# Performance work log

Hardware: AMD Instinct MI355X
Metric: run time of the kernel (lower is better)

## Reference

```python
import jax, jax.numpy as jnp
import numpy as np

N = 32768
LAYERS = [3, 128, 128, 128, 128, 128, 128, 128, 128, 2]


def setup_inputs() -> dict:
    key = jax.random.key(0)
    keys = jax.random.split(key, 3 + 2 * (len(LAYERS) - 1))
    inp = {
        "x": jax.random.normal(keys[0], (N, 1), jnp.float32),
        "y": jax.random.normal(keys[1], (N, 1), jnp.float32),
        "t": jax.random.normal(keys[2], (N, 1), jnp.float32),
    }
    # torch.nn.Linear default init: U(-1/sqrt(fan_in), 1/sqrt(fan_in))
    for i in range(len(LAYERS) - 1):
        bound = 1.0 / np.sqrt(LAYERS[i])
        inp[f"W{i}"] = jax.random.uniform(keys[3 + 2 * i], (LAYERS[i], LAYERS[i + 1]), jnp.float32, -bound, bound)
        inp[f"b{i}"] = jax.random.uniform(keys[4 + 2 * i], (LAYERS[i + 1],), jnp.float32, -bound, bound)
    inp["lam1"] = jnp.asarray([1.0], jnp.float32)
    inp["lam2"] = jnp.asarray([0.01], jnp.float32)
    return inp


def _pinn(x, y, t, params, lam1, lam2):
    pts = jnp.concatenate([x, y, t], axis=1)  # [N,3], columns = (x, y, t)

    def psi(pt):  # pt: [3] -> scalar stream function (output column 0)
        h = pt
        for W, b in params:
            h = jnp.tanh(h @ W + b)  # note: tanh applied to last layer too, as in source
        return h[0]

    g_fn = jax.grad(psi)          # [3]        d psi / d(x,y,t)
    H_fn = jax.jacfwd(g_fn)       # [3,3]      second derivatives
    T_fn = jax.jacfwd(H_fn)       # [3,3,3]    third derivatives
    g, H, T = jax.vmap(lambda pt: (g_fn(pt), H_fn(pt), T_fn(pt)))(pts)

    col = lambda a: a[:, None]  # [N] -> [N,1]
    u = col(g[:, 1])            # u = psi_y
    v = col(-g[:, 0])           # v = -psi_x
    u_x, u_y, u_t = col(H[:, 1, 0]), col(H[:, 1, 1]), col(H[:, 1, 2])
    v_x, v_y, v_t = col(-H[:, 0, 0]), col(-H[:, 0, 1]), col(-H[:, 0, 2])
    u_xx, u_yy = col(T[:, 1, 0, 0]), col(T[:, 1, 1, 1])
    v_xx, v_yy = col(-T[:, 0, 0, 0]), col(-T[:, 0, 1, 1])

    f_u = u_t + lam1 * (u * u_x + v * u_y) - lam2 * (u_xx + u_yy)
    f_v = v_t + lam1 * (u * v_x + v * v_y) - lam2 * (v_xx + v_yy)
    return u, v, f_u, f_v


def reference(x, y, t, W0, b0, W1, b1, W2, b2, W3, b3, W4, b4, W5, b5, W6, b6, W7, b7, W8, b8, lam1, lam2):
    params = [(W0, b0), (W1, b1), (W2, b2), (W3, b3), (W4, b4), (W5, b5), (W6, b6), (W7, b7), (W8, b8)]
    return _pinn(x, y, t, params, lam1, lam2)
```

## Files before the change

### kernel.cpp

```cpp
#include <hip/hip_runtime.h>
#include <math.h>

#define NPTS 32768
#define HID  128
#define PPB  4
#define NCH  13
#define KB   32

typedef __attribute__((ext_vector_type(8))) _Float16 f16x8;
typedef __attribute__((ext_vector_type(4))) float f32x4;

struct PinnArgs {
  const float* x; const float* y; const float* t;
  const float* W[9]; const float* b[9];
  const float* lam1; const float* lam2;
  float* out;
  const _Float16* wt;
};

struct PrepArgs { const float* W[7]; _Float16* out; };

__device__ __forceinline__ void compose13(const float z[NCH], float o[NCH]) {
  const float v  = tanhf(z[0]);
  const float f1 = 1.f - v * v;
  const float f2 = -2.f * v * f1;
  const float f3 = f1 * (4.f * v * v - 2.f * f1);
  const float gx = z[1], gy = z[2], gt = z[3];
  const float hxx = z[4], hxy = z[5], hxt = z[6], hyy = z[7], hyt = z[8];
  o[0] = v;
  o[1] = f1 * gx; o[2] = f1 * gy; o[3] = f1 * gt;
  o[4] = f2 * gx * gx + f1 * hxx;
  o[5] = f2 * gx * gy + f1 * hxy;
  o[6] = f2 * gx * gt + f1 * hxt;
  o[7] = f2 * gy * gy + f1 * hyy;
  o[8] = f2 * gy * gt + f1 * hyt;
  o[9]  = f3 * gx * gx * gx + f2 * (3.f * hxx * gx)            + f1 * z[9];
  o[10] = f3 * gx * gx * gy + f2 * (hxx * gy + 2.f * hxy * gx) + f1 * z[10];
  o[11] = f3 * gx * gy * gy + f2 * (2.f * hxy * gy + hyy * gx) + f1 * z[11];
  o[12] = f3 * gy * gy * gy + f2 * (3.f * hyy * gy)            + f1 * z[12];
}

__global__ __launch_bounds__(256) void prep_w16(PrepArgs P) {
  const int idx = blockIdx.x * 256 + threadIdx.x;
  if (idx >= 7 * 16384) return;
  const int L = idx >> 14;
  const int r = idx & 16383;
  const int n = r & 127;
  const int k = r >> 7;
  const float w = P.W[L][k * HID + n];
  const _Float16 hi = (_Float16)w;
  const _Float16 lo = (_Float16)(w - (float)hi);
  P.out[(size_t)(L * 2 + 0) * 16384 + n * 128 + k] = hi;
  P.out[(size_t)(L * 2 + 1) * 16384 + n * 128 + k] = lo;
}

__global__ __launch_bounds__(256, 3) void pinn_mfma(PinnArgs A) {
  __shared__ _Float16 Ah[64][136];
  __shared__ _Float16 Al[64][136];
  __shared__ float    Zh[64][68];
  const int tid  = threadIdx.x;
  const int wave = tid >> 6;
  const int lane = tid & 63;
  const int kg   = lane >> 4;
  const int lr   = lane & 15;
  const int pbase = blockIdx.x * PPB;

  if (tid < 136) {
#pragma unroll
    for (int pp = 0; pp < PPB; ++pp)
#pragma unroll
      for (int c = NCH; c < 16; ++c) {
        Ah[pp * 16 + c][tid] = (_Float16)0.f;
        Al[pp * 16 + c][tid] = (_Float16)0.f;
      }
  }

  for (int t = tid; t < PPB * HID; t += 256) {
    const int p = t >> 7, j = t & 127;
    const int gp = pbase + p;
    const float xv = A.x[gp], yv = A.y[gp], tv = A.t[gp];
    const float wx = A.W[0][j], wy = A.W[0][HID + j], wz = A.W[0][2 * HID + j];
    float z[NCH], o[NCH];
    z[0] = fmaf(wx, xv, fmaf(wy, yv, fmaf(wz, tv, A.b[0][j])));
    z[1] = wx; z[2] = wy; z[3] = wz;
#pragma unroll
    for (int c = 4; c < NCH; ++c) z[c] = 0.f;
    compose13(z, o);
#pragma unroll
    for (int c = 0; c < NCH; ++c) {
      const _Float16 hi = (_Float16)o[c];
      Ah[p * 16 + c][j] = hi;
      Al[p * 16 + c][j] = (_Float16)(o[c] - (float)hi);
    }
  }
  __syncthreads();

#pragma unroll 1
  for (int L = 1; L <= 7; ++L) {
    const _Float16* __restrict__ WH = A.wt + (size_t)(L - 1) * 2 * 16384;
    const _Float16* __restrict__ WL = WH + 16384;
    f16x8 bh[2][4], bl[2][4];
#pragma unroll
    for (int nt = 0; nt < 2; ++nt) {
      const int col = wave * 32 + nt * 16 + lr;
#pragma unroll
      for (int ks = 0; ks < 4; ++ks) {
        const int k0 = ks * 32 + kg * 8;
        bh[nt][ks] = *(const f16x8*)(WH + col * 128 + k0);
        bl[nt][ks] = *(const f16x8*)(WL + col * 128 + k0);
      }
    }
    f32x4 acc[4][2];
#pragma unroll
    for (int m = 0; m < 4; ++m)
#pragma unroll
      for (int nt = 0; nt < 2; ++nt) acc[m][nt] = (f32x4)(0.f);

#pragma unroll
    for (int ks = 0; ks < 4; ++ks) {
      const int k0 = ks * 32 + kg * 8;
#pragma unroll
      for (int m = 0; m < 4; ++m) {
        const int row = m * 16 + lr;
        const f16x8 ah = *(const f16x8*)&Ah[row][k0];
        const f16x8 al = *(const f16x8*)&Al[row][k0];
#pragma unroll
        for (int nt = 0; nt < 2; ++nt) {
          acc[m][nt] = __builtin_amdgcn_mfma_f32_16x16x32_f16(ah, bh[nt][ks], acc[m][nt], 0, 0, 0);
          acc[m][nt] = __builtin_amdgcn_mfma_f32_16x16x32_f16(ah, bl[nt][ks], acc[m][nt], 0, 0, 0);
          acc[m][nt] = __builtin_amdgcn_mfma_f32_16x16x32_f16(al, bh[nt][ks], acc[m][nt], 0, 0, 0);
        }
      }
    }

    const float* __restrict__ bb = A.b[L];
#pragma unroll
    for (int nt = 0; nt < 2; ++nt) {
#pragma unroll
      for (int m = 0; m < 4; ++m)
        *(f32x4*)&Zh[wave * 16 + lr][m * 16 + kg * 4] = acc[m][nt];
      __syncthreads();

      {
        const int p = wave;
        const int s = lane;
        const int j = ((s >> 4) << 5) + nt * 16 + (s & 15);
        float zf[16], o[NCH];
#pragma unroll
        for (int q = 0; q < 4; ++q)
          ((f32x4*)zf)[q] = *(const f32x4*)&Zh[s][p * 16 + 4 * q];
        zf[0] += bb[j];
        compose13(zf, o);
#pragma unroll
        for (int c = 0; c < NCH; ++c) {
          const _Float16 hi = (_Float16)o[c];
          Ah[p * 16 + c][j] = hi;
          Al[p * 16 + c][j] = (_Float16)(o[c] - (float)hi);
        }
      }
      __syncthreads();
    }
  }

  {
    const int p = wave, gp = pbase + p;
    const float w0 = A.W[8][2 * lane];
    const float w1 = A.W[8][2 * (lane + 64)];
    float zc[NCH];
#pragma unroll
    for (int c = 0; c < NCH; ++c) {
      const int rr = p * 16 + c;
      const float s0 = (float)Ah[rr][lane]      + (float)Al[rr][lane];
      const float s1 = (float)Ah[rr][lane + 64] + (float)Al[rr][lane + 64];
      zc[c] = fmaf(s0, w0, s1 * w1);
    }
#pragma unroll
    for (int off = 32; off; off >>= 1) {
#pragma unroll
      for (int c = 0; c < NCH; ++c) zc[c] += __shfl_xor(zc[c], off, 64);
    }
    if (lane == 0) {
      zc[0] += A.b[8][0];
      float o[NCH];
      compose13(zc, o);
      const float u  =  o[2];
      const float vv = -o[1];
      const float ux =  o[5],  uy =  o[7],  ut =  o[8];
      const float vx = -o[4],  vy = -o[5],  vt = -o[6];
      const float uxx =  o[10], uyy =  o[12];
      const float vxx = -o[9],  vyy = -o[11];
      const float l1 = A.lam1[0], l2 = A.lam2[0];
      const float fu = ut + l1 * (u * ux + vv * uy) - l2 * (uxx + uyy);
      const float fv = vt + l1 * (u * vx + vv * vy) - l2 * (vxx + vyy);
      A.out[gp]            = u;
      A.out[NPTS + gp]     = vv;
      A.out[2 * NPTS + gp] = fu;
      A.out[3 * NPTS + gp] = fv;
    }
  }
}

__device__ __forceinline__ void compose20(const float z[20], float o[20]) {
  const float v  = tanhf(z[0]);
  const float f1 = 1.f - v * v;
  const float f2 = -2.f * v * f1;
  const float f3 = f1 * (4.f * v * v - 2.f * f1);
  const float gx = z[1], gy = z[2], gt = z[3];
  const float hxx = z[4], hxy = z[5], hxz = z[6], hyy = z[7], hyz = z[8], hzz = z[9];
  o[0] = v;
  o[1] = f1 * gx; o[2] = f1 * gy; o[3] = f1 * gt;
  o[4] = f2 * gx * gx + f1 * hxx;
  o[5] = f2 * gx * gy + f1 * hxy;
  o[6] = f2 * gx * gt + f1 * hxz;
  o[7] = f2 * gy * gy + f1 * hyy;
  o[8] = f2 * gy * gt + f1 * hyz;
  o[9] = f2 * gt * gt + f1 * hzz;
  o[10] = f3 * gx * gx * gx + f2 * (3.f * hxx * gx)                 + f1 * z[10];
  o[11] = f3 * gx * gx * gy + f2 * (hxx * gy + 2.f * hxy * gx)      + f1 * z[11];
  o[12] = f3 * gx * gx * gt + f2 * (hxx * gt + 2.f * hxz * gx)      + f1 * z[12];
  o[13] = f3 * gx * gy * gy + f2 * (2.f * hxy * gy + hyy * gx)      + f1 * z[13];
  o[14] = f3 * gx * gy * gt + f2 * (hxy * gt + hxz * gy + hyz * gx) + f1 * z[14];
  o[15] = f3 * gx * gt * gt + f2 * (2.f * hxz * gt + hzz * gx)      + f1 * z[15];
  o[16] = f3 * gy * gy * gy + f2 * (3.f * hyy * gy)                 + f1 * z[16];
  o[17] = f3 * gy * gy * gt + f2 * (hyy * gt + 2.f * hyz * gy)      + f1 * z[17];
  o[18] = f3 * gy * gt * gt + f2 * (2.f * hyz * gt + hzz * gy)      + f1 * z[18];
  o[19] = f3 * gt * gt * gt + f2 * (3.f * hzz * gt)                 + f1 * z[19];
}

__global__ __launch_bounds__(256) void pinn_fp32(PinnArgs A) {
  __shared__ float S[4][HID][20];
  __shared__ float Wt[KB][HID];
  const int wave = threadIdx.x >> 6;
  const int lane = threadIdx.x & 63;
  const int p    = blockIdx.x * 4 + wave;
  const int j0   = lane * 2;
  {
    const float xv = A.x[p], yv = A.y[p], tv = A.t[p];
    const float* W0 = A.W[0];
    const float* b0 = A.b[0];
#pragma unroll
    for (int jj = 0; jj < 2; ++jj) {
      const int j = j0 + jj;
      const float wx = W0[j], wy = W0[HID + j], wz = W0[2 * HID + j];
      float z[20];
      z[0] = fmaf(wx, xv, fmaf(wy, yv, fmaf(wz, tv, b0[j])));
      z[1] = wx; z[2] = wy; z[3] = wz;
#pragma unroll
      for (int c = 4; c < 20; ++c) z[c] = 0.f;
      float o[20];
      compose20(z, o);
#pragma unroll
      for (int q = 0; q < 5; ++q)
        *((float4*)&S[wave][j][4 * q]) = ((float4*)o)[q];
    }
  }
#pragma unroll 1
  for (int L = 1; L <= 7; ++L) {
    const float* __restrict__ W = A.W[L];
    float2 acc[20];
#pragma unroll
    for (int c = 0; c < 20; ++c) acc[c] = make_float2(0.f, 0.f);
    for (int kb = 0; kb < HID; kb += KB) {
      __syncthreads();
      const float4* src = (const float4*)(W + kb * HID);
#pragma unroll
      for (int i = 0; i < (KB * HID / 4) / 256; ++i)
        ((float4*)Wt)[threadIdx.x + i * 256] = src[threadIdx.x + i * 256];
      __syncthreads();
#pragma unroll 4
      for (int k = 0; k < KB; ++k) {
        float s[20];
        const float4* srow = (const float4*)&S[wave][kb + k][0];
#pragma unroll
        for (int q = 0; q < 5; ++q) ((float4*)s)[q] = srow[q];
        const float2 w2 = *(const float2*)&Wt[k][j0];
#pragma unroll
        for (int c = 0; c < 20; ++c) {
          acc[c].x = fmaf(s[c], w2.x, acc[c].x);
          acc[c].y = fmaf(s[c], w2.y, acc[c].y);
        }
      }
    }
    const float* b = A.b[L];
    float za[20], zb[20];
#pragma unroll
    for (int c = 0; c < 20; ++c) { za[c] = acc[c].x; zb[c] = acc[c].y; }
    za[0] += b[j0];
    zb[0] += b[j0 + 1];
    float oa[20], ob[20];
    compose20(za, oa);
    compose20(zb, ob);
#pragma unroll
    for (int q = 0; q < 5; ++q) {
      *((float4*)&S[wave][j0][4 * q])     = ((float4*)oa)[q];
      *((float4*)&S[wave][j0 + 1][4 * q]) = ((float4*)ob)[q];
    }
  }
  {
    const float* W8 = A.W[8];
    float zc[20];
#pragma unroll
    for (int c = 0; c < 20; ++c) zc[c] = 0.f;
#pragma unroll
    for (int kk = 0; kk < 2; ++kk) {
      const int k = lane + kk * 64;
      const float w = W8[2 * k];
      float s[20];
      const float4* srow = (const float4*)&S[wave][k][0];
#pragma unroll
      for (int q = 0; q < 5; ++q) ((float4*)s)[q] = srow[q];
#pragma unroll
      for (int c = 0; c < 20; ++c) zc[c] = fmaf(s[c], w, zc[c]);
    }
#pragma unroll
    for (int off = 32; off; off >>= 1) {
#pragma unroll
      for (int c = 0; c < 20; ++c) zc[c] += __shfl_xor(zc[c], off, 64);
    }
    if (lane == 0) {
      zc[0] += A.b[8][0];
      float o[20];
      compose20(zc, o);
      const float u  =  o[2];
      const float vv = -o[1];
      const float ux =  o[5],  uy =  o[7],  ut =  o[8];
      const float vx = -o[4],  vy = -o[5],  vt = -o[6];
      const float uxx =  o[11], uyy =  o[16];
      const float vxx = -o[10], vyy = -o[13];
      const float l1 = A.lam1[0], l2 = A.lam2[0];
      const float fu = ut + l1 * (u * ux + vv * uy) - l2 * (uxx + uyy);
      const float fv = vt + l1 * (u * vx + vv * vy) - l2 * (vxx + vyy);
      A.out[p]            = u;
      A.out[NPTS + p]     = vv;
      A.out[2 * NPTS + p] = fu;
      A.out[3 * NPTS + p] = fv;
    }
  }
}

extern "C" void kernel_launch(void* const* d_in, const int* in_sizes, int n_in,
                              void* d_out, int out_size, void* d_ws, size_t ws_size,
                              hipStream_t stream) {
  PinnArgs A;
  A.x = (const float*)d_in[0];
  A.y = (const float*)d_in[1];
  A.t = (const float*)d_in[2];
  for (int i = 0; i < 9; ++i) {
    A.W[i] = (const float*)d_in[3 + 2 * i];
    A.b[i] = (const float*)d_in[4 + 2 * i];
  }
  A.lam1 = (const float*)d_in[21];
  A.lam2 = (const float*)d_in[22];
  A.out  = (float*)d_out;
  A.wt   = (const _Float16*)d_ws;

  const size_t need = (size_t)7 * 2 * 16384 * sizeof(_Float16);
  if (ws_size >= need) {
    PrepArgs P;
    for (int L = 1; L <= 7; ++L) P.W[L - 1] = (const float*)d_in[3 + 2 * L];
    P.out = (_Float16*)d_ws;
    hipLaunchKernelGGL(prep_w16, dim3((7 * 16384) / 256), dim3(256), 0, stream, P);
    hipLaunchKernelGGL(pinn_mfma, dim3(NPTS / PPB), dim3(256), 0, stream, A);
  } else {
    hipLaunchKernelGGL(pinn_fp32, dim3(NPTS / 4), dim3(256), 0, stream, A);
  }
}
```

Baseline: 527.9 us.

## Retile hidden-layer MFMA as 2x2 wave grid with A fragments held in registers

Each wave now owns a 32-row by 64-column output tile (a 2x2 wave grid) instead of all 64 rows by 32 columns. The A (activation) fragments are loaded from LDS once into registers and reused across four N-tiles. Weight B fragments are streamed per N-tile from global memory. The goal is fewer LDS reads per MFMA and a better balance between LDS and global/L2 traffic. The Zh staging and the column mapping are rewritten to match the new ownership, which changes register pressure.

```diff
diff --git a/kernel.cpp b/kernel.cpp
--- a/kernel.cpp
+++ b/kernel.cpp
@@ -63,6 +63,8 @@
   const int lane = tid & 63;
   const int kg   = lane >> 4;
   const int lr   = lane & 15;
+  const int mw   = wave >> 1;
+  const int nw   = wave & 1;
   const int pbase = blockIdx.x * PPB;
 
   if (tid < 136) {
@@ -99,56 +101,64 @@
   for (int L = 1; L <= 7; ++L) {
     const _Float16* __restrict__ WH = A.wt + (size_t)(L - 1) * 2 * 16384;
     const _Float16* __restrict__ WL = WH + 16384;
-    f16x8 bh[2][4], bl[2][4];
-#pragma unroll
-    for (int nt = 0; nt < 2; ++nt) {
-      const int col = wave * 32 + nt * 16 + lr;
+
+    f16x8 afh[2][4], afl[2][4];
+#pragma unroll
+    for (int m = 0; m < 2; ++m)
+#pragma unroll
+      for (int ks = 0; ks < 4; ++ks) {
+        const int row = mw * 32 + m * 16 + lr;
+        const int k0  = ks * 32 + kg * 8;
+        afh[m][ks] = *(const f16x8*)&Ah[row][k0];
+        afl[m][ks] = *(const f16x8*)&Al[row][k0];
+      }
+
+    f32x4 acc[2][4];
+#pragma unroll
+    for (int m = 0; m < 2; ++m)
+#pragma unroll
+      for (int nt = 0; nt < 4; ++nt) acc[m][nt] = (f32x4)(0.f);
+
+#pragma unroll
+    for (int nt = 0; nt < 4; ++nt) {
+      const int col = nw * 64 + nt * 16 + lr;
+      f16x8 bh[4], bl[4];
 #pragma unroll
       for (int ks = 0; ks < 4; ++ks) {
         const int k0 = ks * 32 + kg * 8;
-        bh[nt][ks] = *(const f16x8*)(WH + col * 128 + k0);
-        bl[nt][ks] = *(const f16x8*)(WL + col * 128 + k0);
-      }
-    }
-    f32x4 acc[4][2];
-#pragma unroll
-    for (int m = 0; m < 4; ++m)
-#pragma unroll
-      for (int nt = 0; nt < 2; ++nt) acc[m][nt] = (f32x4)(0.f);
-
-#pragma unroll
-    for (int ks = 0; ks < 4; ++ks) {
-      const int k0 = ks * 32 + kg * 8;
-#pragma unroll
-      for (int m = 0; m < 4; ++m) {
-        const int row = m * 16 + lr;
-        const f16x8 ah = *(const f16x8*)&Ah[row][k0];
-        const f16x8 al = *(const f16x8*)&Al[row][k0];
-#pragma unroll
-        for (int nt = 0; nt < 2; ++nt) {
-          acc[m][nt] = __builtin_amdgcn_mfma_f32_16x16x32_f16(ah, bh[nt][ks], acc[m][nt], 0, 0, 0);
-          acc[m][nt] = __builtin_amdgcn_mfma_f32_16x16x32_f16(ah, bl[nt][ks], acc[m][nt], 0, 0, 0);
-          acc[m][nt] = __builtin_amdgcn_mfma_f32_16x16x32_f16(al, bh[nt][ks], acc[m][nt], 0, 0, 0);
+        bh[ks] = *(const f16x8*)(WH + col * 128 + k0);
+        bl[ks] = *(const f16x8*)(WL + col * 128 + k0);
+      }
+#pragma unroll
+      for (int ks = 0; ks < 4; ++ks)
+#pragma unroll
+        for (int m = 0; m < 2; ++m) {
+          acc[m][nt] = __builtin_amdgcn_mfma_f32_16x16x32_f16(afh[m][ks], bh[ks], acc[m][nt], 0, 0, 0);
+          acc[m][nt] = __builtin_amdgcn_mfma_f32_16x16x32_f16(afh[m][ks], bl[ks], acc[m][nt], 0, 0, 0);
+          acc[m][nt] = __builtin_amdgcn_mfma_f32_16x16x32_f16(afl[m][ks], bh[ks], acc[m][nt], 0, 0, 0);
         }
-      }
     }
 
     const float* __restrict__ bb = A.b[L];
 #pragma unroll
-    for (int nt = 0; nt < 2; ++nt) {
-#pragma unroll
-      for (int m = 0; m < 4; ++m)
-        *(f32x4*)&Zh[wave * 16 + lr][m * 16 + kg * 4] = acc[m][nt];
+    for (int s = 0; s < 2; ++s) {
+#pragma unroll
+      for (int m = 0; m < 2; ++m)
+#pragma unroll
+        for (int i = 0; i < 2; ++i) {
+          const int cs = nw * 32 + i * 16 + lr;
+          *(f32x4*)&Zh[cs][mw * 32 + m * 16 + kg * 4] = acc[m][2 * s + i];
+        }
       __syncthreads();
 
       {
-        const int p = wave;
-        const int s = lane;
-        const int j = ((s >> 4) << 5) + nt * 16 + (s & 15);
+        const int p  = wave;
+        const int cs = lane;
+        const int j  = ((cs >> 5) << 6) + s * 32 + (cs & 31);
         float zf[16], o[NCH];
 #pragma unroll
         for (int q = 0; q < 4; ++q)
-          ((f32x4*)zf)[q] = *(const f32x4*)&Zh[s][p * 16 + 4 * q];
+          ((f32x4*)zf)[q] = *(const f32x4*)&Zh[cs][p * 16 + 4 * q];
         zf[0] += bb[j];
         compose13(zf, o);
 #pragma unroll
```

Result: slower. 851.7 us (+61.3%).
